# Performance work log

Measured on AMD Instinct MI355X. Metric: run time of the kernel, lower is better.

## Reference

```python
import jax, jax.numpy as jnp
import numpy as np

B, N, D, H = 2, 2048, 1024, 16
HD = D // H  # head_dim = 64


def l2norm(x, eps=1e-12):
    n = jnp.sqrt(jnp.sum(x * x, axis=-1, keepdims=True))
    return x / jnp.maximum(n, eps)


def setup_inputs() -> dict:
    key = jax.random.key(0)
    ks = jax.random.split(key, 10)
    s = 0.02
    return {
        "x": jax.random.normal(ks[0], (B, N, D), jnp.float32),
        "Wq": jax.random.normal(ks[1], (D, D), jnp.float32) * s,
        "Wk": jax.random.normal(ks[2], (D, D), jnp.float32) * s,
        "Wv": jax.random.normal(ks[3], (D, D), jnp.float32) * s,
        "Wgamma": jax.random.normal(ks[4], (D, H), jnp.float32) * s,
        "Wf": jax.random.normal(ks[5], (D, H), jnp.float32) * s,
        "Wg1": jax.random.normal(ks[6], (D, HD), jnp.float32) * s,
        "Wg2": jax.random.normal(ks[7], (HD, D), jnp.float32) * s,
        "Wo": jax.random.normal(ks[8], (D, D), jnp.float32) * s,
        "norm_w": jnp.ones((D,), jnp.float32),
    }


def dplr_delta_rule(q, k, v, a, gk):
    # q,k,v,a,gk: (B,N,H,HD). State S: (B,H,Dk,Dv). b-vector == k here.
    # S' = S * exp(gk_t); S_t = S' + k_t (x) (a_t @ S' + v_t); o_t = q_t @ S_t
    qm, km, vm, am, gm = (jnp.moveaxis(t, 1, 0) for t in (q, k, v, a, gk))

    def step(S, inp):
        qt, kt, vt, at, gkt = inp  # (B,H,HD)
        Sp = S * jnp.exp(gkt)[..., None]
        u = jnp.einsum('bhk,bhkv->bhv', at, Sp) + vt
        S = Sp + jnp.einsum('bhk,bhv->bhkv', kt, u)
        o = jnp.einsum('bhk,bhkv->bhv', qt, S)
        return S, o

    S0 = jnp.zeros((q.shape[0], q.shape[2], q.shape[3], v.shape[3]), q.dtype)
    _, o = jax.lax.scan(step, S0, (qm, km, vm, am, gm))
    return jnp.moveaxis(o, 0, 1)  # (B,N,H,HD)


def _forward(x, Wq, Wk, Wv, Wgamma, Wf, Wg1, Wg2, Wo, norm_w):
    b, n, d = x.shape
    silu = jax.nn.silu
    q = silu(x @ Wq)
    k = silu(x @ Wk)
    v = silu(x @ Wv)
    log_f = jax.nn.log_sigmoid(x @ Wf)          # (b,n,H) scalar decay per head
    gamma = -jax.nn.sigmoid(x @ Wgamma)         # (b,n,H), 'pos' activation
    q = q.reshape(b, n, H, HD)
    k = l2norm(k.reshape(b, n, H, HD))
    v = v.reshape(b, n, H, HD)
    gk = jnp.broadcast_to(log_f[..., None], (b, n, H, HD))  # repeat over head_dim
    a = k * gamma[..., None] * jnp.exp(gk)
    out = dplr_delta_rule(q, k, v, a, gk)       # scale=1
    out = out.reshape(b, n, d)
    gate = jax.nn.sigmoid((x @ Wg1) @ Wg2)
    out = out * gate
    # LayerNorm (weight only, no bias)
    mu = jnp.mean(out, axis=-1, keepdims=True)
    var = jnp.mean(jnp.square(out - mu), axis=-1, keepdims=True)
    out = (out - mu) * jax.lax.rsqrt(var + 1e-5) * norm_w
    return out @ Wo


def reference(x, Wq, Wk, Wv, Wgamma, Wf, Wg1, Wg2, Wo, norm_w):
    return _forward(x, Wq, Wk, Wv, Wgamma, Wf, Wg1, Wg2, Wo, norm_w)
```

## Files before the change

### kernel.cpp

```cpp
#include <hip/hip_runtime.h>

#define BB 2
#define NN 2048
#define DD 1024
#define HH 16
#define HD 64
#define RR (BB * NN)
#define CT 32
#define NC (NN / CT)

typedef __bf16 bf16x8 __attribute__((ext_vector_type(8)));
typedef __bf16 bf16x4 __attribute__((ext_vector_type(4)));
typedef float f32x4 __attribute__((ext_vector_type(4)));
typedef float f32x2 __attribute__((ext_vector_type(2)));

__device__ __forceinline__ float sigmoidf_(float x) { return 1.f / (1.f + __expf(-x)); }

#define MFMA16(a, b, c) __builtin_amdgcn_mfma_f32_16x16x32_bf16((a), (b), (c), 0, 0, 0)

__device__ __forceinline__ void gl2lds16(const void* g, void* l) {
    __builtin_amdgcn_global_load_lds((const __attribute__((address_space(1))) void*)g,
                                     (__attribute__((address_space(3))) void*)l, 16, 0, 0);
}
__device__ __forceinline__ void gl2lds4(const void* g, void* l) {
    __builtin_amdgcn_global_load_lds((const __attribute__((address_space(1))) void*)g,
                                     (__attribute__((address_space(3))) void*)l, 4, 0, 0);
}

__global__ __launch_bounds__(256) void xcvt(const float* __restrict__ x,
                                            __bf16* __restrict__ xb) {
    const size_t i = ((size_t)blockIdx.x * 256 + threadIdx.x) * 8;
    float4 a = *(const float4*)(x + i);
    float4 b = *(const float4*)(x + i + 4);
    bf16x8 o;
    o[0] = (__bf16)a.x; o[1] = (__bf16)a.y; o[2] = (__bf16)a.z; o[3] = (__bf16)a.w;
    o[4] = (__bf16)b.x; o[5] = (__bf16)b.y; o[6] = (__bf16)b.z; o[7] = (__bf16)b.w;
    *(bf16x8*)(xb + i) = o;
}

__global__ __launch_bounds__(256) void wtrans(const float* S0, const float* S1,
                                              const float* S2, const float* S3,
                                              __bf16* D0, __bf16* D1,
                                              __bf16* D2, __bf16* D3,
                                              int K, int N) {
    __shared__ float t[64][65];
    const int z = blockIdx.z;
    const float* S = (z == 0) ? S0 : ((z == 1) ? S1 : ((z == 2) ? S2 : S3));
    __bf16* D = (z == 0) ? D0 : ((z == 1) ? D1 : ((z == 2) ? D2 : D3));
    const int tid = threadIdx.x;
    const int ti = blockIdx.y * 64;
    const int tj = blockIdx.x * 64;
    const int r = tid >> 2, c0 = (tid & 3) * 16;
    const float* sp = S + (size_t)(ti + r) * N + tj + c0;
#pragma unroll
    for (int p = 0; p < 4; p++) {
        float4 v = *(const float4*)(sp + 4 * p);
        t[r][c0 + 4 * p + 0] = v.x; t[r][c0 + 4 * p + 1] = v.y;
        t[r][c0 + 4 * p + 2] = v.z; t[r][c0 + 4 * p + 3] = v.w;
    }
    __syncthreads();
    bf16x8 o0, o1;
#pragma unroll
    for (int j = 0; j < 8; j++) o0[j] = (__bf16)t[c0 + j][r];
#pragma unroll
    for (int j = 0; j < 8; j++) o1[j] = (__bf16)t[c0 + 8 + j][r];
    __bf16* dp = D + (size_t)(tj + r) * K + ti + c0;
    *(bf16x8*)dp = o0;
    *(bf16x8*)(dp + 8) = o1;
}

__global__ __launch_bounds__(256) void wtrans96(const float* __restrict__ Wgm,
                                                const float* __restrict__ Wf,
                                                const float* __restrict__ Wg1,
                                                __bf16* __restrict__ W96T) {
    const int c = blockIdx.x;
    const int k0 = threadIdx.x * 4;
    bf16x4 o;
    if (c < 96) {
        const float* src;
        int stride;
        if (c < 16)      { src = Wgm + c;        stride = 16; }
        else if (c < 32) { src = Wf + (c - 16);  stride = 16; }
        else             { src = Wg1 + (c - 32); stride = 64; }
#pragma unroll
        for (int j = 0; j < 4; j++) o[j] = (__bf16)src[(size_t)(k0 + j) * stride];
    } else {
        o[0] = o[1] = o[2] = o[3] = (__bf16)0.f;
    }
    *(bf16x4*)(W96T + (size_t)c * 1024 + k0) = o;
}

__global__ __launch_bounds__(256) void gemm_bt(const __bf16* __restrict__ A,
                                               const __bf16* B0, const __bf16* B1,
                                               const __bf16* B2, const __bf16* B3,
                                               float* C0, float* C1, float* C2, float* C3,
                                               int M, int N, int K) {
    constexpr int BK = 32;
    __shared__ __align__(16) __bf16 As[128 * BK];
    __shared__ __align__(16) __bf16 Bs[128 * BK];
    const int mat = blockIdx.x >> 3;
    const __bf16* B = (mat == 0) ? B0 : ((mat == 1) ? B1 : ((mat == 2) ? B2 : B3));
    float* C = (mat == 0) ? C0 : ((mat == 1) ? C1 : ((mat == 2) ? C2 : C3));
    const int Nn = (mat == 3) ? 128 : N;
    const int tid = threadIdx.x;
    const int lane = tid & 63;
    const int wave = tid >> 6;
    const int wm = (wave >> 1) * 64, wn = (wave & 1) * 64;
    const int bm = blockIdx.y * 128, bn = (blockIdx.x & 7) * 128;
    const int l15 = lane & 15, quad = lane >> 4;

    const int srow = lane >> 2, scol = (lane & 3) * 8;
    const __bf16* gA = A + (size_t)(bm + wave * 16 + srow) * K + scol;
    const __bf16* gB = B + (size_t)(bn + wave * 16 + srow) * K + scol;
    const size_t rstep = (size_t)64 * K;
    __bf16* lA0 = &As[(wave * 16) * BK];
    __bf16* lA1 = &As[(wave * 16 + 64) * BK];
    __bf16* lB0 = &Bs[(wave * 16) * BK];
    __bf16* lB1 = &Bs[(wave * 16 + 64) * BK];

    f32x4 acc[4][4];
#pragma unroll
    for (int i = 0; i < 4; i++)
#pragma unroll
        for (int j = 0; j < 4; j++) acc[i][j] = (f32x4){0.f, 0.f, 0.f, 0.f};

    for (int kb = 0; kb < K; kb += BK) {
        gl2lds16(gA + kb, lA0);
        gl2lds16(gA + kb + rstep, lA1);
        gl2lds16(gB + kb, lB0);
        gl2lds16(gB + kb + rstep, lB1);
        asm volatile("s_waitcnt vmcnt(0)" ::: "memory");
        __syncthreads();

        bf16x8 af[4], bfr[4];
#pragma unroll
        for (int i = 0; i < 4; i++)
            af[i] = *(const bf16x8*)&As[(wm + i * 16 + l15) * BK + quad * 8];
#pragma unroll
        for (int j = 0; j < 4; j++)
            bfr[j] = *(const bf16x8*)&Bs[(wn + j * 16 + l15) * BK + quad * 8];
#pragma unroll
        for (int i = 0; i < 4; i++)
#pragma unroll
            for (int j = 0; j < 4; j++)
                acc[i][j] = MFMA16(af[i], bfr[j], acc[i][j]);
        __syncthreads();
    }

#pragma unroll
    for (int i = 0; i < 4; i++) {
#pragma unroll
        for (int r = 0; r < 4; r++) {
            const int row = bm + wm + i * 16 + quad * 4 + r;
            float* cp = C + (size_t)row * Nn + bn + wn + l15;
#pragma unroll
            for (int j = 0; j < 4; j++) cp[j * 16] = acc[i][j][r];
        }
    }
}

__global__ __launch_bounds__(256) void prep_kernel(float* qb, float* kb, float* vb,
                                                   const float* __restrict__ c96,
                                                   float* lfb, float* csb,
                                                   __bf16* __restrict__ g1b) {
    const int tid = threadIdx.x;
    const int wav = tid >> 6, lane = tid & 63;
    const int gid = blockIdx.x * 4 + wav;
    const int r = gid >> 4, h = gid & 15;
    const size_t idx = (size_t)r * DD + (size_t)h * HD + lane;

    float xq = qb[idx], xk = kb[idx], xv = vb[idx];
    float q = xq * sigmoidf_(xq);
    float v = xv * sigmoidf_(xv);
    float kk = xk * sigmoidf_(xk);
    float ss = kk * kk;
#pragma unroll
    for (int m = 1; m <= 32; m <<= 1) ss += __shfl_xor(ss, m);
    float norm = fmaxf(sqrtf(ss), 1e-12f);
    float kn = kk / norm;

    float f = c96[(size_t)r * 128 + 16 + h];
    float sig = sigmoidf_(f);
    float gm = -sigmoidf_(c96[(size_t)r * 128 + h]);

    qb[idx] = q;
    vb[idx] = v;
    kb[idx] = kn;
    if (lane == 0) {
        lfb[(size_t)r * HH + h] = sig;
        csb[(size_t)r * HH + h] = gm * sig * sig;
    }
    if (h == 0) g1b[(size_t)r * 64 + lane] = (__bf16)c96[(size_t)r * 128 + 32 + lane];
}

__global__ __launch_bounds__(64) void chunk_prep(const float* __restrict__ qb,
                                                 const float* __restrict__ kb,
                                                 const float* __restrict__ lfb,
                                                 const float* __restrict__ csb,
                                                 __bf16* __restrict__ ck_hat,
                                                 __bf16* __restrict__ ck_q,
                                                 __bf16* __restrict__ ck_kbT,
                                                 __bf16* __restrict__ ck_M,
                                                 __bf16* __restrict__ ck_G,
                                                 float* __restrict__ ck_lam) {
    __shared__ __align__(16) __bf16 khL[32][72];
    __shared__ __align__(16) __bf16 kbL[32][72];
    __shared__ __align__(16) __bf16 qtL[32][72];
    __shared__ float Afp[32][33];
    __shared__ float scl[3][32];
    const int bx = blockIdx.x;
    const int bh = bx >> 6, ci = bx & 63;
    const int b = bh >> 4, h = bh & 15;
    const int l = threadIdx.x;
    const int l15 = l & 15, quad = l >> 4, t32 = l & 31;
    const size_t cid = (size_t)bh * NC + ci;

    const size_t mb = ((size_t)(b * NN + ci * CT) + t32) * HH + h;
    float c_t = csb[mb];
    float p = lfb[mb];
#pragma unroll
    for (int d = 1; d <= 16; d <<= 1) {
        float o = __shfl_up(p, d);
        p *= (t32 >= d) ? o : 1.f;
    }
    float pm1 = __shfl_up(p, 1);
    if (t32 == 0) pm1 = 1.f;
    const float lamT = __shfl(p, 31);
    if (l < 32) {
        scl[0][t32] = c_t * pm1;
        scl[1][t32] = 1.f / p;
        scl[2][t32] = p;
    }
    if (l == 0) ck_lam[cid] = lamT;
    __syncthreads();

    const size_t rb0 = ((size_t)(b * NN + ci * CT)) * DD + h * HD;
    __bf16* khG = ck_hat + cid * 2048;
    __bf16* qtG = ck_q + cid * 2048;
    __bf16* kTG = ck_kbT + cid * 2048;
#pragma unroll
    for (int rep = 0; rep < 8; rep++) {
        const int row = rep * 4 + quad;
        const int c4 = l15 * 4;
        float4 kv = *(const float4*)(kb + rb0 + (size_t)row * DD + c4);
        float4 qv = *(const float4*)(qb + rb0 + (size_t)row * DD + c4);
        const float sh = scl[0][row], sbr = scl[1][row], sq = scl[2][row];
        bf16x4 khv, kbv, qtv;
        khv[0] = (__bf16)(kv.x * sh); khv[1] = (__bf16)(kv.y * sh);
        khv[2] = (__bf16)(kv.z * sh); khv[3] = (__bf16)(kv.w * sh);
        kbv[0] = (__bf16)(kv.x * sbr); kbv[1] = (__bf16)(kv.y * sbr);
        kbv[2] = (__bf16)(kv.z * sbr); kbv[3] = (__bf16)(kv.w * sbr);
        qtv[0] = (__bf16)(qv.x * sq); qtv[1] = (__bf16)(qv.y * sq);
        qtv[2] = (__bf16)(qv.z * sq); qtv[3] = (__bf16)(qv.w * sq);
        *(bf16x4*)&khL[row][c4] = khv;
        *(bf16x4*)&kbL[row][c4] = kbv;
        *(bf16x4*)&qtL[row][c4] = qtv;
        *(bf16x4*)(khG + row * 64 + c4) = khv;
        *(bf16x4*)(qtG + row * 64 + c4) = qtv;
#pragma unroll
        for (int j = 0; j < 4; j++) kTG[(c4 + j) * 32 + row] = kbv[j];
    }
    __syncthreads();

    __bf16* GG = ck_G + cid * 1024;
#pragma unroll
    for (int mi = 0; mi < 2; mi++)
#pragma unroll
        for (int ni = 0; ni < 2; ni++) {
            f32x4 aA = (f32x4){0.f, 0.f, 0.f, 0.f};
            f32x4 aG = (f32x4){0.f, 0.f, 0.f, 0.f};
#pragma unroll
            for (int k2 = 0; k2 < 2; k2++) {
                bf16x8 bfr = *(const bf16x8*)&kbL[ni * 16 + l15][k2 * 32 + quad * 8];
                bf16x8 afr = *(const bf16x8*)&khL[mi * 16 + l15][k2 * 32 + quad * 8];
                bf16x8 qfr = *(const bf16x8*)&qtL[mi * 16 + l15][k2 * 32 + quad * 8];
                aA = MFMA16(afr, bfr, aA);
                aG = MFMA16(qfr, bfr, aG);
            }
#pragma unroll
            for (int r = 0; r < 4; r++) {
                const int row = mi * 16 + quad * 4 + r, col = ni * 16 + l15;
                Afp[row][col] = (col < row) ? aA[r] : 0.f;
                GG[row * 32 + col] = (__bf16)((col <= row) ? aG[r] : 0.f);
            }
        }
    __syncthreads();

    __bf16* MG = ck_M + cid * 1024;
    if (l < 32) {
        float m[32];
#pragma unroll
        for (int t = 0; t < 32; t++) {
            float r = (l == t) ? 1.f : 0.f;
#pragma unroll
            for (int s = 0; s < t; s++) r += Afp[t][s] * m[s];
            m[t] = r;
            MG[t * 32 + l] = (__bf16)r;
        }
    }
}

struct FragSet {
    bf16x8 ka[2][2], qa[2][2], ma[2], ga[2], kba[4];
    f32x4 vv[2];
    float lam;
};

__global__ __launch_bounds__(64) void chunk_scan(const __bf16* __restrict__ ck_hat,
                                                 const __bf16* __restrict__ ck_q,
                                                 const __bf16* __restrict__ ck_kbT,
                                                 const __bf16* __restrict__ ck_M,
                                                 const __bf16* __restrict__ ck_G,
                                                 const float* __restrict__ ck_lam,
                                                 const float* __restrict__ vb,
                                                 __bf16* __restrict__ obh) {
    __shared__ __align__(16) __bf16 Sbt[16][72];
    __shared__ __align__(16) __bf16 Vbt[16][40];
    __shared__ __align__(16) __bf16 Ubt[16][40];
    const int bx = blockIdx.x;
    const int bh = bx >> 2, vs = bx & 3;
    const int b = bh >> 4, h = bh & 15;
    const int l = threadIdx.x, l15 = l & 15, quad = l >> 4;
    const size_t cid0 = (size_t)bh * NC;
    const size_t vcol = (size_t)h * HD + vs * 16 + l15;
    const size_t rowb = (size_t)b * NN;

    f32x4 S[4];
#pragma unroll
    for (int dt = 0; dt < 4; dt++) S[dt] = (f32x4){0.f, 0.f, 0.f, 0.f};

    auto load = [&](FragSet& f, int ci) {
        const __bf16* khp = ck_hat + (cid0 + ci) * 2048;
        const __bf16* qp = ck_q + (cid0 + ci) * 2048;
        const __bf16* kTp = ck_kbT + (cid0 + ci) * 2048;
        const __bf16* Mp = ck_M + (cid0 + ci) * 1024;
        const __bf16* Gp = ck_G + (cid0 + ci) * 1024;
#pragma unroll
        for (int mi = 0; mi < 2; mi++) {
#pragma unroll
            for (int k2 = 0; k2 < 2; k2++) {
                f.ka[mi][k2] = *(const bf16x8*)(khp + (mi * 16 + l15) * 64 + k2 * 32 + quad * 8);
                f.qa[mi][k2] = *(const bf16x8*)(qp + (mi * 16 + l15) * 64 + k2 * 32 + quad * 8);
            }
            f.ma[mi] = *(const bf16x8*)(Mp + (mi * 16 + l15) * 32 + quad * 8);
            f.ga[mi] = *(const bf16x8*)(Gp + (mi * 16 + l15) * 32 + quad * 8);
        }
#pragma unroll
        for (int dt = 0; dt < 4; dt++)
            f.kba[dt] = *(const bf16x8*)(kTp + (dt * 16 + l15) * 32 + quad * 8);
#pragma unroll
        for (int mi = 0; mi < 2; mi++)
#pragma unroll
            for (int r = 0; r < 4; r++)
                f.vv[mi][r] = vb[(rowb + ci * CT + mi * 16 + quad * 4 + r) * DD + vcol];
        f.lam = ck_lam[cid0 + ci];
    };

    auto compute = [&](const FragSet& f, int ci) {
        const f32x4 z = (f32x4){0.f, 0.f, 0.f, 0.f};
#pragma unroll
        for (int dt = 0; dt < 4; dt++) {
            bf16x4 t;
#pragma unroll
            for (int r = 0; r < 4; r++) t[r] = (__bf16)S[dt][r];
            *(bf16x4*)&Sbt[l15][dt * 16 + quad * 4] = t;
        }
        bf16x8 sb0 = *(const bf16x8*)&Sbt[l15][quad * 8];
        bf16x8 sb1 = *(const bf16x8*)&Sbt[l15][32 + quad * 8];
        f32x4 p0 = MFMA16(f.ka[0][0], sb0, z); p0 = MFMA16(f.ka[0][1], sb1, p0);
        f32x4 p1 = MFMA16(f.ka[1][0], sb0, z); p1 = MFMA16(f.ka[1][1], sb1, p1);
        p0 += f.vv[0]; p1 += f.vv[1];
        bf16x4 t0, t1;
#pragma unroll
        for (int r = 0; r < 4; r++) { t0[r] = (__bf16)p0[r]; t1[r] = (__bf16)p1[r]; }
        *(bf16x4*)&Vbt[l15][quad * 4] = t0;
        *(bf16x4*)&Vbt[l15][16 + quad * 4] = t1;
        bf16x8 vfr = *(const bf16x8*)&Vbt[l15][quad * 8];
        f32x4 u0 = MFMA16(f.ma[0], vfr, z);
        f32x4 u1 = MFMA16(f.ma[1], vfr, z);
#pragma unroll
        for (int r = 0; r < 4; r++) { t0[r] = (__bf16)u0[r]; t1[r] = (__bf16)u1[r]; }
        *(bf16x4*)&Ubt[l15][quad * 4] = t0;
        *(bf16x4*)&Ubt[l15][16 + quad * 4] = t1;
        bf16x8 ufr = *(const bf16x8*)&Ubt[l15][quad * 8];
        f32x4 o0 = MFMA16(f.qa[0][0], sb0, z); o0 = MFMA16(f.qa[0][1], sb1, o0);
        o0 = MFMA16(f.ga[0], ufr, o0);
        f32x4 o1 = MFMA16(f.qa[1][0], sb0, z); o1 = MFMA16(f.qa[1][1], sb1, o1);
        o1 = MFMA16(f.ga[1], ufr, o1);
#pragma unroll
        for (int r = 0; r < 4; r++) {
            obh[(rowb + ci * CT + quad * 4 + r) * DD + vcol] = (__bf16)o0[r];
            obh[(rowb + ci * CT + 16 + quad * 4 + r) * DD + vcol] = (__bf16)o1[r];
        }
#pragma unroll
        for (int dt = 0; dt < 4; dt++) {
            S[dt] = MFMA16(f.kba[dt], ufr, S[dt]);
#pragma unroll
            for (int r = 0; r < 4; r++) S[dt][r] *= f.lam;
        }
    };

    FragSet fA, fB;
    load(fA, 0);
    for (int ci = 0; ci < NC; ci += 2) {
        load(fB, ci + 1);
        __builtin_amdgcn_sched_barrier(0);
        compute(fA, ci);
        load(fA, (ci + 2 < NC) ? ci + 2 : NC - 1);
        __builtin_amdgcn_sched_barrier(0);
        compute(fB, ci + 1);
    }
}

__global__ __launch_bounds__(256) void gate_ln_kernel(const __bf16* __restrict__ obh,
                                                      const float* __restrict__ gatep,
                                                      const float* __restrict__ nw,
                                                      __bf16* __restrict__ lnob) {
    const int r = blockIdx.x, tid = threadIdx.x;
    const int wav = tid >> 6, lane = tid & 63;
    __shared__ float red[8];
    const size_t rb = (size_t)r * DD;

    float vals[4];
    float s = 0.f;
#pragma unroll
    for (int p = 0; p < 4; p++) {
        const int j = tid + 256 * p;
        float xg = (float)obh[rb + j] * sigmoidf_(gatep[rb + j]);
        vals[p] = xg;
        s += xg;
    }
#pragma unroll
    for (int m = 1; m <= 32; m <<= 1) s += __shfl_xor(s, m);
    if (lane == 0) red[wav] = s;
    __syncthreads();
    const float mu = (red[0] + red[1] + red[2] + red[3]) * (1.f / 1024.f);

    float s2 = 0.f;
#pragma unroll
    for (int p = 0; p < 4; p++) { float d = vals[p] - mu; s2 += d * d; }
#pragma unroll
    for (int m = 1; m <= 32; m <<= 1) s2 += __shfl_xor(s2, m);
    if (lane == 0) red[4 + wav] = s2;
    __syncthreads();
    const float var = (red[4] + red[5] + red[6] + red[7]) * (1.f / 1024.f);
    const float rs = rsqrtf(var + 1e-5f);

#pragma unroll
    for (int p = 0; p < 4; p++) {
        const int j = tid + 256 * p;
        lnob[rb + j] = (__bf16)((vals[p] - mu) * rs * nw[j]);
    }
}

extern "C" void kernel_launch(void* const* d_in, const int* in_sizes, int n_in,
                              void* d_out, int out_size, void* d_ws, size_t ws_size,
                              hipStream_t stream) {
    const float* x   = (const float*)d_in[0];
    const float* Wq  = (const float*)d_in[1];
    const float* Wk  = (const float*)d_in[2];
    const float* Wv  = (const float*)d_in[3];
    const float* Wgm = (const float*)d_in[4];
    const float* Wf  = (const float*)d_in[5];
    const float* Wg1 = (const float*)d_in[6];
    const float* Wg2 = (const float*)d_in[7];
    const float* Wo  = (const float*)d_in[8];
    const float* nw  = (const float*)d_in[9];
    float* out = (float*)d_out;

    float* w = (float*)d_ws;
    float* qb    = w;
    float* kb    = qb + 4194304;
    float* vb    = kb + 4194304;
    float* gatep = vb + 4194304;
    __bf16* g1b  = (__bf16*)(gatep + 4194304);
    float* lfb   = gatep + 4194304 + 131072;
    float* csb   = lfb + 65536;
    __bf16* obh  = (__bf16*)(csb + 65536);
    float* cw    = csb + 65536 + 2097152;
    __bf16* ck_hat = (__bf16*)cw;
    __bf16* ck_q   = (__bf16*)(cw + 2097152);
    __bf16* ck_kbT = (__bf16*)(cw + 4194304);
    __bf16* ck_M   = (__bf16*)(cw + 6291456);
    __bf16* ck_G   = (__bf16*)(cw + 7340032);
    float*  ck_lam = cw + 8388608;
    float* nw2   = cw + 8390656;
    __bf16* xb   = (__bf16*)nw2;
    __bf16* WqT  = (__bf16*)(nw2 + 2097152);
    __bf16* WkT  = (__bf16*)(nw2 + 2621440);
    __bf16* WvT  = (__bf16*)(nw2 + 3145728);
    __bf16* WoT  = (__bf16*)(nw2 + 3670016);
    __bf16* Wg2T = (__bf16*)(nw2 + 4194304);
    __bf16* W96T = (__bf16*)(nw2 + 4227072);
    float* c96   = nw2 + 4292608;
    __bf16* lnob = (__bf16*)qb;

    dim3 blk(256);
    xcvt<<<2048, blk, 0, stream>>>(x, xb);
    wtrans<<<dim3(16, 16, 4), blk, 0, stream>>>(Wq, Wk, Wv, Wo, WqT, WkT, WvT, WoT,
                                                DD, DD);
    wtrans<<<dim3(16, 1, 1), blk, 0, stream>>>(Wg2, Wg2, Wg2, Wg2, Wg2T, Wg2T, Wg2T,
                                               Wg2T, HD, DD);
    wtrans96<<<128, blk, 0, stream>>>(Wgm, Wf, Wg1, W96T);
    gemm_bt<<<dim3(25, 32), blk, 0, stream>>>(xb, WqT, WkT, WvT, W96T,
                                              qb, kb, vb, c96, RR, DD, DD);
    prep_kernel<<<RR * HH / 4, blk, 0, stream>>>(qb, kb, vb, c96, lfb, csb, g1b);
    gemm_bt<<<dim3(8, 32), blk, 0, stream>>>(g1b, Wg2T, Wg2T, Wg2T, Wg2T,
                                             gatep, gatep, gatep, gatep, RR, DD, HD);
    chunk_prep<<<32 * NC, 64, 0, stream>>>(qb, kb, lfb, csb,
                                           ck_hat, ck_q, ck_kbT, ck_M, ck_G, ck_lam);
    chunk_scan<<<128, 64, 0, stream>>>(ck_hat, ck_q, ck_kbT, ck_M, ck_G, ck_lam, vb, obh);
    gate_ln_kernel<<<RR, blk, 0, stream>>>(obh, gatep, nw, lnob);
    gemm_bt<<<dim3(8, 32), blk, 0, stream>>>(lnob, WoT, WoT, WoT, WoT,
                                             out, out, out, out, RR, DD, DD);
}
```

Baseline: 281.9 us.

## Fuse SiLU/L2norm into chunk kernels and prefetch next GEMM K-tile

Removes the elementwise prep pass over q/k/v (a full read and write of three RR×DD fp32 tensors). SiLU and the per-row L2 norm of k now happen inside chunk_prep, and SiLU of v happens when chunk_scan loads it, leaving only a small scalar prep kernel. The GEMM main loop is also changed so the global-to-LDS load of the next K tile is issued after fragments are read into registers, overlapping it with the MFMAs. The cost is extra sigmoid work recomputed in the consumer kernels, plus an added barrier per iteration.

```diff
diff --git a/kernel.cpp b/kernel.cpp
--- a/kernel.cpp
+++ b/kernel.cpp
@@ -21,10 +21,6 @@
 __device__ __forceinline__ void gl2lds16(const void* g, void* l) {
     __builtin_amdgcn_global_load_lds((const __attribute__((address_space(1))) void*)g,
                                      (__attribute__((address_space(3))) void*)l, 16, 0, 0);
-}
-__device__ __forceinline__ void gl2lds4(const void* g, void* l) {
-    __builtin_amdgcn_global_load_lds((const __attribute__((address_space(1))) void*)g,
-                                     (__attribute__((address_space(3))) void*)l, 4, 0, 0);
 }
 
 __global__ __launch_bounds__(256) void xcvt(const float* __restrict__ x,
@@ -124,11 +120,12 @@
 #pragma unroll
         for (int j = 0; j < 4; j++) acc[i][j] = (f32x4){0.f, 0.f, 0.f, 0.f};
 
+    gl2lds16(gA, lA0);
+    gl2lds16(gA + rstep, lA1);
+    gl2lds16(gB, lB0);
+    gl2lds16(gB + rstep, lB1);
+
     for (int kb = 0; kb < K; kb += BK) {
-        gl2lds16(gA + kb, lA0);
-        gl2lds16(gA + kb + rstep, lA1);
-        gl2lds16(gB + kb, lB0);
-        gl2lds16(gB + kb + rstep, lB1);
         asm volatile("s_waitcnt vmcnt(0)" ::: "memory");
         __syncthreads();
 
@@ -139,12 +136,21 @@
 #pragma unroll
         for (int j = 0; j < 4; j++)
             bfr[j] = *(const bf16x8*)&Bs[(wn + j * 16 + l15) * BK + quad * 8];
+        __syncthreads();
+
+        if (kb + BK < K) {
+            gl2lds16(gA + kb + BK, lA0);
+            gl2lds16(gA + kb + BK + rstep, lA1);
+            gl2lds16(gB + kb + BK, lB0);
+            gl2lds16(gB + kb + BK + rstep, lB1);
+        }
+        __builtin_amdgcn_sched_barrier(0);
+
 #pragma unroll
         for (int i = 0; i < 4; i++)
 #pragma unroll
             for (int j = 0; j < 4; j++)
                 acc[i][j] = MFMA16(af[i], bfr[j], acc[i][j]);
-        __syncthreads();
     }
 
 #pragma unroll
@@ -159,38 +165,23 @@
     }
 }
 
-__global__ __launch_bounds__(256) void prep_kernel(float* qb, float* kb, float* vb,
-                                                   const float* __restrict__ c96,
-                                                   float* lfb, float* csb,
-                                                   __bf16* __restrict__ g1b) {
+__global__ __launch_bounds__(256) void scal_prep(const float* __restrict__ c96,
+                                                 float* __restrict__ lfb,
+                                                 float* __restrict__ csb,
+                                                 __bf16* __restrict__ g1b) {
     const int tid = threadIdx.x;
-    const int wav = tid >> 6, lane = tid & 63;
-    const int gid = blockIdx.x * 4 + wav;
-    const int r = gid >> 4, h = gid & 15;
-    const size_t idx = (size_t)r * DD + (size_t)h * HD + lane;
-
-    float xq = qb[idx], xk = kb[idx], xv = vb[idx];
-    float q = xq * sigmoidf_(xq);
-    float v = xv * sigmoidf_(xv);
-    float kk = xk * sigmoidf_(xk);
-    float ss = kk * kk;
-#pragma unroll
-    for (int m = 1; m <= 32; m <<= 1) ss += __shfl_xor(ss, m);
-    float norm = fmaxf(sqrtf(ss), 1e-12f);
-    float kn = kk / norm;
-
-    float f = c96[(size_t)r * 128 + 16 + h];
-    float sig = sigmoidf_(f);
-    float gm = -sigmoidf_(c96[(size_t)r * 128 + h]);
-
-    qb[idx] = q;
-    vb[idx] = v;
-    kb[idx] = kn;
-    if (lane == 0) {
-        lfb[(size_t)r * HH + h] = sig;
-        csb[(size_t)r * HH + h] = gm * sig * sig;
-    }
-    if (h == 0) g1b[(size_t)r * 64 + lane] = (__bf16)c96[(size_t)r * 128 + 32 + lane];
+    const int row = blockIdx.x * 16 + (tid >> 4);
+    const int h = tid & 15;
+    const float* cr = c96 + (size_t)row * 128;
+    const float sig = sigmoidf_(cr[16 + h]);
+    const float gm = -sigmoidf_(cr[h]);
+    lfb[(size_t)row * HH + h] = sig;
+    csb[(size_t)row * HH + h] = gm * sig * sig;
+    const int c4 = h * 4;
+    bf16x4 o;
+    o[0] = (__bf16)cr[32 + c4 + 0]; o[1] = (__bf16)cr[32 + c4 + 1];
+    o[2] = (__bf16)cr[32 + c4 + 2]; o[3] = (__bf16)cr[32 + c4 + 3];
+    *(bf16x4*)(g1b + (size_t)row * 64 + c4) = o;
 }
 
 __global__ __launch_bounds__(64) void chunk_prep(const float* __restrict__ qb,
@@ -244,7 +235,15 @@
         const int c4 = l15 * 4;
         float4 kv = *(const float4*)(kb + rb0 + (size_t)row * DD + c4);
         float4 qv = *(const float4*)(qb + rb0 + (size_t)row * DD + c4);
-        const float sh = scl[0][row], sbr = scl[1][row], sq = scl[2][row];
+        kv.x *= sigmoidf_(kv.x); kv.y *= sigmoidf_(kv.y);
+        kv.z *= sigmoidf_(kv.z); kv.w *= sigmoidf_(kv.w);
+        qv.x *= sigmoidf_(qv.x); qv.y *= sigmoidf_(qv.y);
+        qv.z *= sigmoidf_(qv.z); qv.w *= sigmoidf_(qv.w);
+        float ss = kv.x * kv.x + kv.y * kv.y + kv.z * kv.z + kv.w * kv.w;
+        ss += __shfl_xor(ss, 1); ss += __shfl_xor(ss, 2);
+        ss += __shfl_xor(ss, 4); ss += __shfl_xor(ss, 8);
+        const float inv = 1.f / fmaxf(sqrtf(ss), 1e-12f);
+        const float sh = scl[0][row] * inv, sbr = scl[1][row] * inv, sq = scl[2][row];
         bf16x4 khv, kbv, qtv;
         khv[0] = (__bf16)(kv.x * sh); khv[1] = (__bf16)(kv.y * sh);
         khv[2] = (__bf16)(kv.z * sh); khv[3] = (__bf16)(kv.w * sh);
@@ -351,8 +350,10 @@
 #pragma unroll
         for (int mi = 0; mi < 2; mi++)
 #pragma unroll
-            for (int r = 0; r < 4; r++)
-                f.vv[mi][r] = vb[(rowb + ci * CT + mi * 16 + quad * 4 + r) * DD + vcol];
+            for (int r = 0; r < 4; r++) {
+                const float rv = vb[(rowb + ci * CT + mi * 16 + quad * 4 + r) * DD + vcol];
+                f.vv[mi][r] = rv * sigmoidf_(rv);
+            }
         f.lam = ck_lam[cid0 + ci];
     };
 
@@ -504,7 +505,7 @@
     wtrans96<<<128, blk, 0, stream>>>(Wgm, Wf, Wg1, W96T);
     gemm_bt<<<dim3(25, 32), blk, 0, stream>>>(xb, WqT, WkT, WvT, W96T,
                                               qb, kb, vb, c96, RR, DD, DD);
-    prep_kernel<<<RR * HH / 4, blk, 0, stream>>>(qb, kb, vb, c96, lfb, csb, g1b);
+    scal_prep<<<RR / 16, blk, 0, stream>>>(c96, lfb, csb, g1b);
     gemm_bt<<<dim3(8, 32), blk, 0, stream>>>(g1b, Wg2T, Wg2T, Wg2T, Wg2T,
                                              gatep, gatep, gatep, gatep, RR, DD, HD);
     chunk_prep<<<32 * NC, 64, 0, stream>>>(qb, kb, lfb, csb,
```

New measurement: 319.2 us. +13.2%, slower.
